# Performance work log

Measured on AMD Instinct MI355X. Metric: run time of the kernel, lower is better.

The kernel has to match this reference:

```python
import jax, jax.numpy as jnp
import numpy as np

N_NODES = 50000
N_EDGES = 400000


def setup_inputs() -> dict:
    key = jax.random.key(0)
    k1, k2, k3, k4 = jax.random.split(key, 4)
    in_feat = jax.random.normal(k1, (2, 64, 4, N_NODES), dtype=jnp.float32)
    src = jax.random.randint(k2, (N_EDGES,), 0, N_NODES, dtype=jnp.int32)
    dst = jax.random.randint(k3, (N_EDGES,), 0, N_NODES, dtype=jnp.int32)
    W = jax.random.normal(k4, (64, 64), dtype=jnp.float32) * (1.0 / 8.0)
    b = jnp.zeros((64,), dtype=jnp.float32)
    return {"in_feat": in_feat, "src": src, "dst": dst, "W": W, "b": b}


def reference(in_feat, src, dst, W, b):
    # in_feat: (B, h, T, N). Net permutation [3,1,2,0] then [0,3,2,1] == [3,0,2,1]
    x = jnp.transpose(in_feat, (3, 0, 2, 1))  # (N, B, T, h) -- node-major for GraphConv
    N = x.shape[0]
    ones_e = jnp.ones(src.shape[0], dtype=x.dtype)
    deg_out = jnp.clip(jax.ops.segment_sum(ones_e, src, num_segments=N), 1.0)
    deg_in = jnp.clip(jax.ops.segment_sum(ones_e, dst, num_segments=N), 1.0)
    # DGL GraphConv, norm='both', in_feats == out_feats -> aggregate then matmul
    x = x * jax.lax.rsqrt(deg_out)[:, None, None, None]
    agg = jax.ops.segment_sum(x[src], dst, num_segments=N)  # (N, B, T, h)
    agg = agg * jax.lax.rsqrt(deg_in)[:, None, None, None]
    h = jnp.einsum('nbth,hf->nbtf', agg, W) + b
    h = jax.nn.relu(h)
    # inverse permutation [0,3,2,1] then [3,1,2,0] == transpose(h, (1,3,2,0))
    out = jnp.transpose(h, (1, 3, 2, 0))  # (B, h, T, N)
    return jax.nn.relu(out)
```

## Files before the change

kernel.cpp:

```cpp
#include <hip/hip_runtime.h>
#include <hip/hip_fp16.h>


extern "C" __global__ void k_zero(int* __restrict__ p, int n) {
  int i = blockIdx.x * blockDim.x + threadIdx.x;
  if (i < n) p[i] = 0;
}

extern "C" __global__ void k_deg(const int* __restrict__ src, const int* __restrict__ dst,
                                 int* __restrict__ deg_out, int* __restrict__ deg_in, int E) {
  int e = blockIdx.x * blockDim.x + threadIdx.x;
  if (e < E) {
    atomicAdd(&deg_out[src[e]], 1);
    atomicAdd(&deg_in[dst[e]], 1);
  }
}

extern "C" __global__ void k_rsqrt(const int* __restrict__ dgo, const int* __restrict__ dgi,
                                   float* __restrict__ rs_out, float* __restrict__ rs_in, int N) {
  int i = blockIdx.x * blockDim.x + threadIdx.x;
  if (i < N) {
    int a = dgo[i] > 1 ? dgo[i] : 1;
    int b = dgi[i] > 1 ? dgi[i] : 1;
    rs_out[i] = rsqrtf((float)a);
    rs_in[i]  = rsqrtf((float)b);
  }
}

extern "C" __global__ __launch_bounds__(256) void k_scan1(const int* __restrict__ deg,
                                                          int* __restrict__ bsum, int N) {
  __shared__ int red[256];
  int tid = threadIdx.x;
  int i = blockIdx.x * 256 + tid;
  red[tid] = (i < N) ? deg[i] : 0;
  __syncthreads();
  #pragma unroll
  for (int off = 128; off > 0; off >>= 1) {
    if (tid < off) red[tid] += red[tid + off];
    __syncthreads();
  }
  if (tid == 0) bsum[blockIdx.x] = red[0];
}

extern "C" __global__ __launch_bounds__(256) void k_scan2(const int* __restrict__ bsum,
                                                          int* __restrict__ boffs,
                                                          int* __restrict__ offs, int M, int N) {
  __shared__ int sc[256];
  int tid = threadIdx.x;
  int v = (tid < M) ? bsum[tid] : 0;
  sc[tid] = v;
  __syncthreads();
  #pragma unroll
  for (int off = 1; off < 256; off <<= 1) {
    int t = sc[tid];
    if (tid >= off) t += sc[tid - off];
    __syncthreads();
    sc[tid] = t;
    __syncthreads();
  }
  boffs[tid] = sc[tid] - v;
  if (tid == 255) offs[N] = sc[255];
}

extern "C" __global__ __launch_bounds__(256) void k_scan3(const int* __restrict__ deg,
                                                          const int* __restrict__ boffs,
                                                          int* __restrict__ offs, int N) {
  __shared__ int sc[256];
  int tid = threadIdx.x;
  int i = blockIdx.x * 256 + tid;
  int v = (i < N) ? deg[i] : 0;
  sc[tid] = v;
  __syncthreads();
  #pragma unroll
  for (int off = 1; off < 256; off <<= 1) {
    int t = sc[tid];
    if (tid >= off) t += sc[tid - off];
    __syncthreads();
    sc[tid] = t;
    __syncthreads();
  }
  if (i < N) offs[i] = boffs[blockIdx.x] + sc[tid] - v;
}

extern "C" __global__ void k_scatter(const int* __restrict__ src, const int* __restrict__ dst,
                                     const int* __restrict__ offs, int* __restrict__ cursor,
                                     int* __restrict__ csr_src, int E) {
  int e = blockIdx.x * blockDim.x + threadIdx.x;
  if (e < E) {
    int d = dst[e];
    int pos = offs[d] + atomicAdd(&cursor[d], 1);
    csr_src[pos] = src[e];
  }
}

extern "C" __global__ __launch_bounds__(256) void k_transform(
    const float* __restrict__ in_feat, const float* __restrict__ W,
    const float* __restrict__ rs_out, __half* __restrict__ y, int N) {
  int tid = threadIdx.x;
  int wave = tid >> 6, lane = tid & 63;
  int bt = blockIdx.y * 4 + wave;
  int b = bt >> 2, t = bt & 3;
  int fh = blockIdx.z * 32;
  int n = blockIdx.x * 64 + lane;

  const float* xp = in_feat + (size_t)(b * 256 + t) * (size_t)N;
  size_t hstride = (size_t)4 * (size_t)N;

  float acc[32];
  #pragma unroll
  for (int f = 0; f < 32; ++f) acc[f] = 0.0f;

  bool ok = (n < N);

  float xcur[4], xnxt[4];
  #pragma unroll
  for (int u = 0; u < 4; ++u)
    xcur[u] = ok ? xp[(size_t)u * hstride + n] : 0.0f;

  #pragma unroll 1
  for (int h0 = 0; h0 < 60; h0 += 4) {
    #pragma unroll
    for (int u = 0; u < 4; ++u)
      xnxt[u] = ok ? xp[(size_t)(h0 + 4 + u) * hstride + n] : 0.0f;
    #pragma unroll
    for (int u = 0; u < 4; ++u) {
      const float* wrow = W + (h0 + u) * 64 + fh;
      #pragma unroll
      for (int f = 0; f < 32; ++f) acc[f] = fmaf(xcur[u], wrow[f], acc[f]);
    }
    #pragma unroll
    for (int u = 0; u < 4; ++u) xcur[u] = xnxt[u];
  }
  #pragma unroll
  for (int u = 0; u < 4; ++u) {
    const float* wrow = W + (60 + u) * 64 + fh;
    #pragma unroll
    for (int f = 0; f < 32; ++f) acc[f] = fmaf(xcur[u], wrow[f], acc[f]);
  }

  if (ok) {
    float rs = rs_out[n];
    union { unsigned int u[16]; uint4 v[4]; } pk;
    #pragma unroll
    for (int q = 0; q < 16; ++q) {
      __half2 h2 = __float22half2_rn(make_float2(acc[2 * q] * rs, acc[2 * q + 1] * rs));
      pk.u[q] = *(unsigned int*)&h2;
    }
    uint4* yp = (uint4*)(y + (size_t)n * 512 + bt * 64 + fh);
    #pragma unroll
    for (int q = 0; q < 4; ++q) yp[q] = pk.v[q];
  }
}

extern "C" __global__ __launch_bounds__(512) void k_aggregate(
    const __half* __restrict__ y, const int* __restrict__ offs,
    const int* __restrict__ csr_src, const float* __restrict__ rs_in,
    const float* __restrict__ bvec, float* __restrict__ out, int N) {
  __shared__ float agg[16 * 513];
  int tid = threadIdx.x;
  int lane = tid & 63, wave = tid >> 6;
  int n0 = blockIdx.x * 16;

#define ACC_EDGE(s)                                                          \
  {                                                                          \
    const uint4* rp = (const uint4*)(y + (size_t)(s) * 512);                 \
    uint4 u = rp[lane];                                                      \
    float2 f;                                                                \
    f = __half22float2(*(const __half2*)&u.x); accA.x += f.x; accA.y += f.y; \
    f = __half22float2(*(const __half2*)&u.y); accA.z += f.x; accA.w += f.y; \
    f = __half22float2(*(const __half2*)&u.z); accB.x += f.x; accB.y += f.y; \
    f = __half22float2(*(const __half2*)&u.w); accB.z += f.x; accB.w += f.y; \
  }

  #pragma unroll
  for (int k = 0; k < 2; ++k) {
    int nl = k * 8 + wave;
    int n = n0 + nl;
    float4 accA = {0.f, 0.f, 0.f, 0.f};
    float4 accB = {0.f, 0.f, 0.f, 0.f};
    if (n < N) {
      int j0 = offs[n], j1 = offs[n + 1];
      for (int base = j0; base < j1; base += 64) {
        int idxv = csr_src[base + lane];
        int m = j1 - base; if (m > 64) m = 64;
        int e = 0;
        for (; e + 7 < m; e += 8) {
          int s0 = __builtin_amdgcn_readlane(idxv, e);
          int s1 = __builtin_amdgcn_readlane(idxv, e + 1);
          int s2 = __builtin_amdgcn_readlane(idxv, e + 2);
          int s3 = __builtin_amdgcn_readlane(idxv, e + 3);
          int s4 = __builtin_amdgcn_readlane(idxv, e + 4);
          int s5 = __builtin_amdgcn_readlane(idxv, e + 5);
          int s6 = __builtin_amdgcn_readlane(idxv, e + 6);
          int s7 = __builtin_amdgcn_readlane(idxv, e + 7);
          ACC_EDGE(s0); ACC_EDGE(s1); ACC_EDGE(s2); ACC_EDGE(s3);
          ACC_EDGE(s4); ACC_EDGE(s5); ACC_EDGE(s6); ACC_EDGE(s7);
        }
        for (; e + 3 < m; e += 4) {
          int s0 = __builtin_amdgcn_readlane(idxv, e);
          int s1 = __builtin_amdgcn_readlane(idxv, e + 1);
          int s2 = __builtin_amdgcn_readlane(idxv, e + 2);
          int s3 = __builtin_amdgcn_readlane(idxv, e + 3);
          ACC_EDGE(s0); ACC_EDGE(s1); ACC_EDGE(s2); ACC_EDGE(s3);
        }
        for (; e < m; ++e) {
          int s0 = __builtin_amdgcn_readlane(idxv, e);
          ACC_EDGE(s0);
        }
      }
    }
    *(float4*)&agg[nl * 513 + lane * 8] = accA;
    *(float4*)&agg[nl * 513 + lane * 8 + 4] = accB;
  }
#undef ACC_EDGE
  __syncthreads();

  int nl = tid & 15;
  int r0 = tid >> 4;
  int n = n0 + nl;
  float rs = (n < N) ? rs_in[n] : 0.0f;
  #pragma unroll 4
  for (int it = 0; it < 16; ++it) {
    int c = it * 32 + r0;
    float v = agg[nl * 513 + c];
    int f = c & 63, bt = c >> 6;
    int b = bt >> 2, t = bt & 3;
    v = v * rs + bvec[f];
    v = fmaxf(v, 0.0f);
    if (n < N) out[(size_t)((b * 64 + f) * 4 + t) * (size_t)N + n] = v;
  }
}

extern "C" void kernel_launch(void* const* d_in, const int* in_sizes, int n_in,
                              void* d_out, int out_size, void* d_ws, size_t ws_size,
                              hipStream_t stream) {
  const float* in_feat = (const float*)d_in[0];
  const int*   src     = (const int*)d_in[1];
  const int*   dst     = (const int*)d_in[2];
  const float* W       = (const float*)d_in[3];
  const float* bvec    = (const float*)d_in[4];
  float* out = (float*)d_out;

  int N = in_sizes[0] / 512;
  int E = in_sizes[1];

  int A  = (N + 64) & ~63;
  int EA = (E + 63) & ~63;
  int M  = (N + 255) / 256;

  int*   deg_out_i = (int*)d_ws;
  int*   deg_in_i  = deg_out_i + A;
  int*   cursor    = deg_in_i + A;
  int*   offs      = cursor + A;
  int*   bsum      = offs + A;
  int*   boffs     = bsum + 256;
  float* rs_out    = (float*)(boffs + 256);
  float* rs_in     = rs_out + A;
  int*   csr_src   = (int*)(rs_in + A);
  __half* y        = (__half*)(csr_src + EA);

  int z = 3 * A;
  hipLaunchKernelGGL(k_zero, dim3((z + 255) / 256), dim3(256), 0, stream, deg_out_i, z);
  hipLaunchKernelGGL(k_deg, dim3((E + 255) / 256), dim3(256), 0, stream,
                     src, dst, deg_out_i, deg_in_i, E);
  hipLaunchKernelGGL(k_rsqrt, dim3((N + 255) / 256), dim3(256), 0, stream,
                     deg_out_i, deg_in_i, rs_out, rs_in, N);
  hipLaunchKernelGGL(k_scan1, dim3(M), dim3(256), 0, stream, deg_in_i, bsum, N);
  hipLaunchKernelGGL(k_scan2, dim3(1), dim3(256), 0, stream, bsum, boffs, offs, M, N);
  hipLaunchKernelGGL(k_scan3, dim3(M), dim3(256), 0, stream, deg_in_i, boffs, offs, N);
  hipLaunchKernelGGL(k_scatter, dim3((E + 255) / 256), dim3(256), 0, stream,
                     src, dst, offs, cursor, csr_src, E);
  hipLaunchKernelGGL(k_transform, dim3((N + 63) / 64, 2, 2), dim3(256), 0, stream,
                     in_feat, W, rs_out, y, N);
  hipLaunchKernelGGL(k_aggregate, dim3((N + 15) / 16), dim3(512), 0, stream,
                     y, offs, csr_src, rs_in, bvec, out, N);
}
```

Measured before the change: 200.6 us.

## Fuse rsqrt into scan, memset degrees, interleave y layout, batch gather loads

The rsqrt computation is merged into the first scan kernel, and the zeroing kernel is replaced by hipMemsetAsync, removing two launches. The transform kernel now writes y in an interleaved layout so that each lane's 16-byte gather in aggregate holds 4 features from one half and 4 from the other. The aggregate writes these to shared memory as two contiguous float4 halves. The aggregate loop issues all gather loads of an unrolled group before accumulating, raising memory-level parallelism at some register cost.

```diff
diff --git a/kernel.cpp b/kernel.cpp
--- a/kernel.cpp
+++ b/kernel.cpp
@@ -1,11 +1,6 @@
 #include <hip/hip_runtime.h>
 #include <hip/hip_fp16.h>
 
-
-extern "C" __global__ void k_zero(int* __restrict__ p, int n) {
-  int i = blockIdx.x * blockDim.x + threadIdx.x;
-  if (i < n) p[i] = 0;
-}
 
 extern "C" __global__ void k_deg(const int* __restrict__ src, const int* __restrict__ dst,
                                  int* __restrict__ deg_out, int* __restrict__ deg_in, int E) {
@@ -16,23 +11,22 @@
   }
 }
 
-extern "C" __global__ void k_rsqrt(const int* __restrict__ dgo, const int* __restrict__ dgi,
-                                   float* __restrict__ rs_out, float* __restrict__ rs_in, int N) {
-  int i = blockIdx.x * blockDim.x + threadIdx.x;
+extern "C" __global__ __launch_bounds__(256) void k_scan1(const int* __restrict__ deg_in,
+                                                          const int* __restrict__ deg_out,
+                                                          int* __restrict__ bsum,
+                                                          float* __restrict__ rs_out,
+                                                          float* __restrict__ rs_in, int N) {
+  __shared__ int red[256];
+  int tid = threadIdx.x;
+  int i = blockIdx.x * 256 + tid;
+  int di = (i < N) ? deg_in[i] : 0;
+  red[tid] = di;
   if (i < N) {
-    int a = dgo[i] > 1 ? dgo[i] : 1;
-    int b = dgi[i] > 1 ? dgi[i] : 1;
+    int a = deg_out[i] > 1 ? deg_out[i] : 1;
+    int b = di > 1 ? di : 1;
     rs_out[i] = rsqrtf((float)a);
     rs_in[i]  = rsqrtf((float)b);
   }
-}
-
-extern "C" __global__ __launch_bounds__(256) void k_scan1(const int* __restrict__ deg,
-                                                          int* __restrict__ bsum, int N) {
-  __shared__ int red[256];
-  int tid = threadIdx.x;
-  int i = blockIdx.x * 256 + tid;
-  red[tid] = (i < N) ? deg[i] : 0;
   __syncthreads();
   #pragma unroll
   for (int off = 128; off > 0; off >>= 1) {
@@ -140,15 +134,18 @@
 
   if (ok) {
     float rs = rs_out[n];
-    union { unsigned int u[16]; uint4 v[4]; } pk;
-    #pragma unroll
-    for (int q = 0; q < 16; ++q) {
-      __half2 h2 = __float22half2_rn(make_float2(acc[2 * q] * rs, acc[2 * q + 1] * rs));
-      pk.u[q] = *(unsigned int*)&h2;
+    __half* rowp = y + (size_t)n * 512;
+    int l0 = (bt & 3) * 16 + (fh >> 2);
+    int hi = (bt >= 4) ? 4 : 0;
+    #pragma unroll
+    for (int q = 0; q < 8; ++q) {
+      __half2 h0 = __float22half2_rn(make_float2(acc[4 * q] * rs, acc[4 * q + 1] * rs));
+      __half2 h1 = __float22half2_rn(make_float2(acc[4 * q + 2] * rs, acc[4 * q + 3] * rs));
+      uint2 u;
+      u.x = *(unsigned int*)&h0;
+      u.y = *(unsigned int*)&h1;
+      *(uint2*)(rowp + (l0 + q) * 8 + hi) = u;
     }
-    uint4* yp = (uint4*)(y + (size_t)n * 512 + bt * 64 + fh);
-    #pragma unroll
-    for (int q = 0; q < 4; ++q) yp[q] = pk.v[q];
   }
 }
 
@@ -161,15 +158,14 @@
   int lane = tid & 63, wave = tid >> 6;
   int n0 = blockIdx.x * 16;
 
-#define ACC_EDGE(s)                                                          \
+#define LDE(i, s) uint4 u##i = ((const uint4*)(y + (size_t)(s) * 512))[lane];
+#define ADE(i)                                                               \
   {                                                                          \
-    const uint4* rp = (const uint4*)(y + (size_t)(s) * 512);                 \
-    uint4 u = rp[lane];                                                      \
     float2 f;                                                                \
-    f = __half22float2(*(const __half2*)&u.x); accA.x += f.x; accA.y += f.y; \
-    f = __half22float2(*(const __half2*)&u.y); accA.z += f.x; accA.w += f.y; \
-    f = __half22float2(*(const __half2*)&u.z); accB.x += f.x; accB.y += f.y; \
-    f = __half22float2(*(const __half2*)&u.w); accB.z += f.x; accB.w += f.y; \
+    f = __half22float2(*(const __half2*)&u##i.x); accA.x += f.x; accA.y += f.y; \
+    f = __half22float2(*(const __half2*)&u##i.y); accA.z += f.x; accA.w += f.y; \
+    f = __half22float2(*(const __half2*)&u##i.z); accB.x += f.x; accB.y += f.y; \
+    f = __half22float2(*(const __half2*)&u##i.w); accB.z += f.x; accB.w += f.y; \
   }
 
   #pragma unroll
@@ -193,26 +189,29 @@
           int s5 = __builtin_amdgcn_readlane(idxv, e + 5);
           int s6 = __builtin_amdgcn_readlane(idxv, e + 6);
           int s7 = __builtin_amdgcn_readlane(idxv, e + 7);
-          ACC_EDGE(s0); ACC_EDGE(s1); ACC_EDGE(s2); ACC_EDGE(s3);
-          ACC_EDGE(s4); ACC_EDGE(s5); ACC_EDGE(s6); ACC_EDGE(s7);
+          LDE(0, s0); LDE(1, s1); LDE(2, s2); LDE(3, s3);
+          LDE(4, s4); LDE(5, s5); LDE(6, s6); LDE(7, s7);
+          ADE(0); ADE(1); ADE(2); ADE(3); ADE(4); ADE(5); ADE(6); ADE(7);
         }
         for (; e + 3 < m; e += 4) {
           int s0 = __builtin_amdgcn_readlane(idxv, e);
           int s1 = __builtin_amdgcn_readlane(idxv, e + 1);
           int s2 = __builtin_amdgcn_readlane(idxv, e + 2);
           int s3 = __builtin_amdgcn_readlane(idxv, e + 3);
-          ACC_EDGE(s0); ACC_EDGE(s1); ACC_EDGE(s2); ACC_EDGE(s3);
+          LDE(0, s0); LDE(1, s1); LDE(2, s2); LDE(3, s3);
+          ADE(0); ADE(1); ADE(2); ADE(3);
         }
         for (; e < m; ++e) {
           int s0 = __builtin_amdgcn_readlane(idxv, e);
-          ACC_EDGE(s0);
+          LDE(0, s0); ADE(0);
         }
       }
     }
-    *(float4*)&agg[nl * 513 + lane * 8] = accA;
-    *(float4*)&agg[nl * 513 + lane * 8 + 4] = accB;
-  }
-#undef ACC_EDGE
+    *(float4*)&agg[nl * 513 + lane * 4] = accA;
+    *(float4*)&agg[nl * 513 + 256 + lane * 4] = accB;
+  }
+#undef LDE
+#undef ADE
   __syncthreads();
 
   int nl = tid & 15;
@@ -259,13 +258,11 @@
   int*   csr_src   = (int*)(rs_in + A);
   __half* y        = (__half*)(csr_src + EA);
 
-  int z = 3 * A;
-  hipLaunchKernelGGL(k_zero, dim3((z + 255) / 256), dim3(256), 0, stream, deg_out_i, z);
+  hipMemsetAsync(deg_out_i, 0, (size_t)(3 * A) * sizeof(int), stream);
   hipLaunchKernelGGL(k_deg, dim3((E + 255) / 256), dim3(256), 0, stream,
                      src, dst, deg_out_i, deg_in_i, E);
-  hipLaunchKernelGGL(k_rsqrt, dim3((N + 255) / 256), dim3(256), 0, stream,
-                     deg_out_i, deg_in_i, rs_out, rs_in, N);
-  hipLaunchKernelGGL(k_scan1, dim3(M), dim3(256), 0, stream, deg_in_i, bsum, N);
+  hipLaunchKernelGGL(k_scan1, dim3(M), dim3(256), 0, stream,
+                     deg_in_i, deg_out_i, bsum, rs_out, rs_in, N);
   hipLaunchKernelGGL(k_scan2, dim3(1), dim3(256), 0, stream, bsum, boffs, offs, M, N);
   hipLaunchKernelGGL(k_scan3, dim3(M), dim3(256), 0, stream, deg_in_i, boffs, offs, N);
   hipLaunchKernelGGL(k_scatter, dim3((E + 255) / 256), dim3(256), 0, stream,
```

New measurement: 214.6 us. +7.0%, slower.
